# Optimization experiments

Hardware: AMD Instinct MI355X
Metric: run time of the kernel (lower is better)

Reference implementation:

```python
import jax, jax.numpy as jnp
import numpy as np
import math

B, S, D, H = 16, 1024, 768, 8
DK = D // H


def setup_inputs() -> dict:
    key = jax.random.key(0)
    ks = jax.random.split(key, 12)
    scale = 1.0 / math.sqrt(D)
    inp = {
        "query": jax.random.normal(ks[0], (B, S, D), jnp.float32),
        "key": jax.random.normal(ks[1], (B, S, D), jnp.float32),
        "value": jax.random.normal(ks[2], (B, S, D), jnp.float32),
        # 4 structured group masks (between/self/global/question), 0/1
        "mask": jax.random.randint(ks[3], (B, 4, S, S), 0, 2, jnp.int32),
        "Wq": jax.random.normal(ks[4], (D, D), jnp.float32) * scale,
        "bq": jnp.zeros((D,), jnp.float32),
        "Wk": jax.random.normal(ks[5], (D, D), jnp.float32) * scale,
        "bk": jnp.zeros((D,), jnp.float32),
        "Wv": jax.random.normal(ks[6], (D, D), jnp.float32) * scale,
        "bv": jnp.zeros((D,), jnp.float32),
        "Wo": jax.random.normal(ks[7], (D, D), jnp.float32) * scale,
        "bo": jnp.zeros((D,), jnp.float32),
    }
    return inp


def _split_heads(x):  # [B,S,D] -> [B,H,S,DK]
    b, s, _ = x.shape
    return x.reshape(b, s, H, DK).transpose(0, 2, 1, 3)


def reference(query, key, value, mask, Wq, bq, Wk, bk, Wv, bv, Wo, bo):
    # mask is 4-D -> torch code concatenates it with itself along dim 1: [B,8,S,S]
    m = jnp.concatenate([mask, mask], axis=1)
    q = _split_heads(query @ Wq.T + bq)
    k = _split_heads(key @ Wk.T + bk)
    v = _split_heads(value @ Wv.T + bv)
    scores = jnp.einsum("bhqd,bhkd->bhqk", q, k) / math.sqrt(DK)
    scores = jnp.where(m == 0, jnp.float32(-1e9), scores)
    p = jax.nn.softmax(scores, axis=-1)  # dropout = identity (eval mode)
    x = jnp.einsum("bhqk,bhkd->bhqd", p, v)
    x = x.transpose(0, 2, 1, 3).reshape(query.shape[0], -1, H * DK)
    return x @ Wo.T + bo
```

## Files before the change

kernel.cpp:

```cpp
#include <hip/hip_runtime.h>
#include <hip/hip_bf16.h>

typedef unsigned short u16;
typedef unsigned long long u64;
typedef __attribute__((ext_vector_type(4))) float f32x4;
typedef __attribute__((ext_vector_type(8))) short s16x8;

constexpr int Sdim = 1024;
constexpr int Hh   = 8;
constexpr int DKc  = 96;
constexpr int Dd   = 768;
constexpr int Bb   = 16;

static __device__ __forceinline__ u16 f2bf(float f) {
    unsigned u = __builtin_bit_cast(unsigned, f);
    u += 0x7fff + ((u >> 16) & 1);
    return (u16)(u >> 16);
}

__global__ __launch_bounds__(256) void convw_kernel(
    const float* w0, const float* w1, const float* w2, const float* w3, u16* dst)
{
    const float* src = (blockIdx.y == 0) ? w0 : (blockIdx.y == 1) ? w1
                      : (blockIdx.y == 2) ? w2 : w3;
    u16* d = dst + (size_t)blockIdx.y * 589824;
    int i = (blockIdx.x * 256 + threadIdx.x) * 4;
    float4 v = *(const float4*)(src + i);
    ushort4 o;
    o.x = f2bf(v.x); o.y = f2bf(v.y); o.z = f2bf(v.z); o.w = f2bf(v.w);
    *(ushort4*)(d + i) = o;
}

__global__ __launch_bounds__(256) void maskpack_kernel(const int* mask, unsigned* packed)
{
    const size_t total  = (size_t)Bb * 4 * Sdim * Sdim;
    const size_t stride = (size_t)gridDim.x * 256;
    const int lane = threadIdx.x & 63;
    for (size_t i = (size_t)blockIdx.x * 256 + threadIdx.x; i < total; i += stride) {
        int mv = mask[i];
        u64 bal = __ballot(mv != 0);
        size_t w0 = (i - lane) >> 5;
        if (lane == 0)  packed[w0]     = (unsigned)bal;
        if (lane == 32) packed[w0 + 1] = (unsigned)(bal >> 32);
    }
}

template<bool QKV>
__global__ __launch_bounds__(256) void gemm_kernel(
    const float* q_f32, const float* k_f32, const float* v_f32,
    const u16* xb, const u16* wb,
    const float* bq, const float* bk, const float* bv, const float* bo,
    u16* qb, u16* kb, u16* vtb, float* out, int Ktot)
{
    constexpr int LDT = 72;
    __shared__ u16 As[128][LDT];
    __shared__ u16 Bs[128][LDT];

    const int z = QKV ? (int)blockIdx.z : 3;
    const float* Af = QKV ? (z == 0 ? q_f32 : z == 1 ? k_f32 : v_f32) : nullptr;
    const u16*   Ab = QKV ? nullptr : xb;
    const u16*   W  = wb + (size_t)(QKV ? z : 3) * 589824;
    const float* bias = QKV ? (z == 0 ? bq : z == 1 ? bk : bv) : bo;

    const int tid = threadIdx.x;
    const int lane = tid & 63;
    const int w = tid >> 6;
    const int wr = (w >> 1) * 64, wc = (w & 1) * 64;
    const int m0 = blockIdx.y * 128, n0 = blockIdx.x * 128;

    f32x4 acc[4][4] = {};

    for (int k0 = 0; k0 < Ktot; k0 += 64) {
        __syncthreads();
        if constexpr (QKV) {
            #pragma unroll
            for (int i = 0; i < 8; i++) {
                int c = tid + i * 256;
                int row = c >> 4, o4 = (c & 15) * 4;
                float4 v = *(const float4*)(Af + (size_t)(m0 + row) * Ktot + k0 + o4);
                ushort4 o;
                o.x = f2bf(v.x); o.y = f2bf(v.y); o.z = f2bf(v.z); o.w = f2bf(v.w);
                *(ushort4*)&As[row][o4] = o;
            }
        } else {
            #pragma unroll
            for (int i = 0; i < 4; i++) {
                int c = tid + i * 256;
                int row = c >> 3, o8 = (c & 7) * 8;
                *(int4*)&As[row][o8] =
                    *(const int4*)(Ab + (size_t)(m0 + row) * Ktot + k0 + o8);
            }
        }
        #pragma unroll
        for (int i = 0; i < 4; i++) {
            int c = tid + i * 256;
            int row = c >> 3, o8 = (c & 7) * 8;
            *(int4*)&Bs[row][o8] =
                *(const int4*)(W + (size_t)(n0 + row) * Ktot + k0 + o8);
        }
        __syncthreads();
        #pragma unroll
        for (int kk = 0; kk < 2; kk++) {
            s16x8 a[4], b[4];
            #pragma unroll
            for (int mi = 0; mi < 4; mi++)
                a[mi] = *(const s16x8*)&As[wr + mi * 16 + (lane & 15)][kk * 32 + (lane >> 4) * 8];
            #pragma unroll
            for (int ni = 0; ni < 4; ni++)
                b[ni] = *(const s16x8*)&Bs[wc + ni * 16 + (lane & 15)][kk * 32 + (lane >> 4) * 8];
            #pragma unroll
            for (int mi = 0; mi < 4; mi++)
                #pragma unroll
                for (int ni = 0; ni < 4; ni++)
                    acc[mi][ni] = __builtin_amdgcn_mfma_f32_16x16x32_bf16(
                        a[mi], b[ni], acc[mi][ni], 0, 0, 0);
        }
    }

    #pragma unroll
    for (int mi = 0; mi < 4; mi++) {
        #pragma unroll
        for (int ni = 0; ni < 4; ni++) {
            int nc = n0 + wc + ni * 16 + (lane & 15);
            int mr0 = m0 + wr + mi * 16 + (lane >> 4) * 4;
            float bvv = bias[nc];
            float vals[4];
            #pragma unroll
            for (int r = 0; r < 4; r++) vals[r] = acc[mi][ni][r] + bvv;

            if constexpr (!QKV) {
                #pragma unroll
                for (int r = 0; r < 4; r++)
                    out[(size_t)(mr0 + r) * Dd + nc] = vals[r];
            } else {
                int b_ = mr0 >> 10, s_ = mr0 & 1023;
                int h_ = nc / DKc, dk = nc - h_ * DKc;
                if (z == 2) {
                    ushort4 o;
                    o.x = f2bf(vals[0]); o.y = f2bf(vals[1]);
                    o.z = f2bf(vals[2]); o.w = f2bf(vals[3]);
                    *(ushort4*)&vtb[((size_t)(b_ * Hh + h_) * DKc + dk) * Sdim + s_] = o;
                } else {
                    u16* dst = (z == 0) ? qb : kb;
                    #pragma unroll
                    for (int r = 0; r < 4; r++)
                        dst[((size_t)(b_ * Hh + h_) * Sdim + (s_ + r)) * DKc + dk] = f2bf(vals[r]);
                }
            }
        }
    }
}

__global__ __launch_bounds__(256) void attn_kernel(
    const u16* qb, const u16* kb, const u16* vtb, const unsigned* mpacked, u16* xb)
{
    __shared__ u16 kbuf[64][104];
    __shared__ u16 vbuf[96][72];
    __shared__ u16 pbuf[4][16][72];

    const int tid = threadIdx.x;
    const int lane = tid & 63;
    const int w = tid >> 6;
    const int bh = blockIdx.y;
    const int b_ = bh >> 3, h_ = bh & 7, g_ = h_ & 3;
    const int q0 = blockIdx.x * 64;

    const u16* Qp = qb + (size_t)bh * Sdim * DKc;
    const u16* Kp = kb + (size_t)bh * Sdim * DKc;
    const u16* Vp = vtb + (size_t)bh * DKc * Sdim;
    const unsigned* Pm = mpacked + (((size_t)(b_ * 4 + g_) * Sdim * Sdim) >> 5);

    #pragma unroll
    for (int i = 0; i < 3; i++) {
        int c = tid + i * 256;
        int row = c / 12, o = (c % 12) * 8;
        *(int4*)&kbuf[row][o] = *(const int4*)(Qp + (size_t)(q0 + row) * DKc + o);
    }
    __syncthreads();
    s16x8 qf[3];
    #pragma unroll
    for (int kk = 0; kk < 3; kk++)
        qf[kk] = *(const s16x8*)&kbuf[w * 16 + (lane & 15)][kk * 32 + (lane >> 4) * 8];
    __syncthreads();

    float m_run[4], l_run[4];
    f32x4 acc[6];
    #pragma unroll
    for (int r = 0; r < 4; r++) { m_run[r] = -1e30f; l_run[r] = 0.f; }
    #pragma unroll
    for (int n2 = 0; n2 < 6; n2++) acc[n2] = (f32x4){0.f, 0.f, 0.f, 0.f};

    const float sc = 0.10206207261596575f;
    const int qrow = q0 + w * 16 + (lane >> 4) * 4;

    for (int kt = 0; kt < 16; kt++) {
        const int kb0 = kt * 64;
        __syncthreads();
        #pragma unroll
        for (int i = 0; i < 3; i++) {
            int c = tid + i * 256;
            int row = c / 12, o = (c % 12) * 8;
            *(int4*)&kbuf[row][o] = *(const int4*)(Kp + (size_t)(kb0 + row) * DKc + o);
        }
        #pragma unroll
        for (int i = 0; i < 3; i++) {
            int c = tid + i * 256;
            int row = c >> 3, o = (c & 7) * 8;
            *(int4*)&vbuf[row][o] = *(const int4*)(Vp + (size_t)row * Sdim + kb0 + o);
        }
        __syncthreads();

        float s[4][4];
        #pragma unroll
        for (int ni = 0; ni < 4; ni++) {
            f32x4 c4 = {0.f, 0.f, 0.f, 0.f};
            #pragma unroll
            for (int kk = 0; kk < 3; kk++) {
                s16x8 bfr = *(const s16x8*)&kbuf[ni * 16 + (lane & 15)][kk * 32 + (lane >> 4) * 8];
                c4 = __builtin_amdgcn_mfma_f32_16x16x32_bf16(qf[kk], bfr, c4, 0, 0, 0);
            }
            #pragma unroll
            for (int r = 0; r < 4; r++) s[ni][r] = c4[r] * sc;
        }

        #pragma unroll
        for (int r = 0; r < 4; r++) {
            u64 mbits = *(const u64*)(Pm + (((size_t)(qrow + r) * Sdim + kb0) >> 5));
            #pragma unroll
            for (int ni = 0; ni < 4; ni++)
                if (!((mbits >> (ni * 16 + (lane & 15))) & 1)) s[ni][r] = -1e9f;
        }

        float alpha[4];
        #pragma unroll
        for (int r = 0; r < 4; r++) {
            float tmax = fmaxf(fmaxf(s[0][r], s[1][r]), fmaxf(s[2][r], s[3][r]));
            tmax = fmaxf(tmax, __shfl_xor(tmax, 1));
            tmax = fmaxf(tmax, __shfl_xor(tmax, 2));
            tmax = fmaxf(tmax, __shfl_xor(tmax, 4));
            tmax = fmaxf(tmax, __shfl_xor(tmax, 8));
            float mn = fmaxf(m_run[r], tmax);
            alpha[r] = __expf(m_run[r] - mn);
            m_run[r] = mn;
            float ps = 0.f;
            #pragma unroll
            for (int ni = 0; ni < 4; ni++) {
                float p = __expf(s[ni][r] - mn);
                s[ni][r] = p;
                ps += p;
            }
            ps += __shfl_xor(ps, 1);
            ps += __shfl_xor(ps, 2);
            ps += __shfl_xor(ps, 4);
            ps += __shfl_xor(ps, 8);
            l_run[r] = l_run[r] * alpha[r] + ps;
        }

        #pragma unroll
        for (int ni = 0; ni < 4; ni++)
            #pragma unroll
            for (int r = 0; r < 4; r++)
                pbuf[w][(lane >> 4) * 4 + r][ni * 16 + (lane & 15)] = f2bf(s[ni][r]);
        #pragma unroll
        for (int n2 = 0; n2 < 6; n2++)
            #pragma unroll
            for (int r = 0; r < 4; r++) acc[n2][r] *= alpha[r];
        asm volatile("s_waitcnt lgkmcnt(0)" ::: "memory");

        #pragma unroll
        for (int kk = 0; kk < 2; kk++) {
            s16x8 pf = *(const s16x8*)&pbuf[w][lane & 15][kk * 32 + (lane >> 4) * 8];
            #pragma unroll
            for (int n2 = 0; n2 < 6; n2++) {
                s16x8 vf = *(const s16x8*)&vbuf[n2 * 16 + (lane & 15)][kk * 32 + (lane >> 4) * 8];
                acc[n2] = __builtin_amdgcn_mfma_f32_16x16x32_bf16(pf, vf, acc[n2], 0, 0, 0);
            }
        }
    }

    #pragma unroll
    for (int n2 = 0; n2 < 6; n2++) {
        int dc = h_ * DKc + n2 * 16 + (lane & 15);
        #pragma unroll
        for (int r = 0; r < 4; r++) {
            float val = acc[n2][r] / l_run[r];
            xb[((size_t)(b_ * Sdim) + (qrow + r)) * Dd + dc] = f2bf(val);
        }
    }
}

extern "C" void kernel_launch(void* const* d_in, const int* in_sizes, int n_in,
                              void* d_out, int out_size, void* d_ws, size_t ws_size,
                              hipStream_t stream)
{
    const float* query = (const float*)d_in[0];
    const float* key   = (const float*)d_in[1];
    const float* value = (const float*)d_in[2];
    const int*   mask  = (const int*)d_in[3];
    const float* Wq = (const float*)d_in[4];
    const float* bq = (const float*)d_in[5];
    const float* Wk = (const float*)d_in[6];
    const float* bk = (const float*)d_in[7];
    const float* Wv = (const float*)d_in[8];
    const float* bv = (const float*)d_in[9];
    const float* Wo = (const float*)d_in[10];
    const float* bo = (const float*)d_in[11];
    float* out = (float*)d_out;

    char* ws = (char*)d_ws;
    u16* qb   = (u16*)(ws);
    u16* kb   = (u16*)(ws + 25165824);
    u16* vtb  = (u16*)(ws + 50331648);
    u16* xb   = (u16*)(ws + 75497472);
    u16* wb   = (u16*)(ws + 100663296);
    unsigned* mp = (unsigned*)(ws + 105381888);

    convw_kernel<<<dim3(576, 4), 256, 0, stream>>>(Wq, Wk, Wv, Wo, wb);
    maskpack_kernel<<<dim3(2048), 256, 0, stream>>>(mask, mp);
    gemm_kernel<true><<<dim3(6, 128, 3), 256, 0, stream>>>(
        query, key, value, nullptr, wb, bq, bk, bv, bo, qb, kb, vtb, out, Dd);
    attn_kernel<<<dim3(16, 128), 256, 0, stream>>>(qb, kb, vtb, mp, xb);
    gemm_kernel<false><<<dim3(6, 128, 1), 256, 0, stream>>>(
        nullptr, nullptr, nullptr, xb, wb, bq, bk, bv, bo, qb, kb, vtb, out, Dd);
}
```

Before: 828.4 us.

## Transpose QK^T tile, add lazy softmax rescale, and use direct-to-LDS GEMM loads

The attention kernel now computes S^T via swapped MFMA operands, so each lane owns a single query row. Row max and sum need only two cross-lane shuffles instead of four per row, and each lane loads one 64-bit mask word per tile. Softmax switches to exp2 with a pre-scaled log2e factor, skips accumulator rescaling unless the max grows by more than 8, and packs P to bf16 with v_cvt_pk_bf16_f32. The GEMM loads weight and bf16 activation tiles with global_load_lds into unpadded LDS, which may add bank conflicts on the fragment reads.

```diff
diff --git a/kernel.cpp b/kernel.cpp
--- a/kernel.cpp
+++ b/kernel.cpp
@@ -2,6 +2,7 @@
 #include <hip/hip_bf16.h>
 
 typedef unsigned short u16;
+typedef unsigned int u32;
 typedef unsigned long long u64;
 typedef __attribute__((ext_vector_type(4))) float f32x4;
 typedef __attribute__((ext_vector_type(8))) short s16x8;
@@ -16,6 +17,12 @@
     unsigned u = __builtin_bit_cast(unsigned, f);
     u += 0x7fff + ((u >> 16) & 1);
     return (u16)(u >> 16);
+}
+
+static __device__ __forceinline__ void gload_lds16(const u16* g, u16* l) {
+    __builtin_amdgcn_global_load_lds(
+        (const __attribute__((address_space(1))) u32*)g,
+        (__attribute__((address_space(3))) u32*)l, 16, 0, 0);
 }
 
 __global__ __launch_bounds__(256) void convw_kernel(
@@ -52,9 +59,9 @@
     const float* bq, const float* bk, const float* bv, const float* bo,
     u16* qb, u16* kb, u16* vtb, float* out, int Ktot)
 {
-    constexpr int LDT = 72;
-    __shared__ u16 As[128][LDT];
-    __shared__ u16 Bs[128][LDT];
+    constexpr int LDA = QKV ? 72 : 64;
+    __shared__ u16 As[128][LDA];
+    __shared__ u16 Bs[128][64];
 
     const int z = QKV ? (int)blockIdx.z : 3;
     const float* Af = QKV ? (z == 0 ? q_f32 : z == 1 ? k_f32 : v_f32) : nullptr;
@@ -72,6 +79,13 @@
 
     for (int k0 = 0; k0 < Ktot; k0 += 64) {
         __syncthreads();
+        #pragma unroll
+        for (int i = 0; i < 4; i++) {
+            int c = (w * 4 + i) * 64 + lane;
+            int row = c >> 3, col = (c & 7) * 8;
+            gload_lds16(W + (size_t)(n0 + row) * Ktot + k0 + col,
+                        ((u16*)Bs) + (size_t)(w * 4 + i) * 512);
+        }
         if constexpr (QKV) {
             #pragma unroll
             for (int i = 0; i < 8; i++) {
@@ -85,18 +99,11 @@
         } else {
             #pragma unroll
             for (int i = 0; i < 4; i++) {
-                int c = tid + i * 256;
-                int row = c >> 3, o8 = (c & 7) * 8;
-                *(int4*)&As[row][o8] =
-                    *(const int4*)(Ab + (size_t)(m0 + row) * Ktot + k0 + o8);
-            }
-        }
-        #pragma unroll
-        for (int i = 0; i < 4; i++) {
-            int c = tid + i * 256;
-            int row = c >> 3, o8 = (c & 7) * 8;
-            *(int4*)&Bs[row][o8] =
-                *(const int4*)(W + (size_t)(n0 + row) * Ktot + k0 + o8);
+                int c = (w * 4 + i) * 64 + lane;
+                int row = c >> 3, col = (c & 7) * 8;
+                gload_lds16(Ab + (size_t)(m0 + row) * Ktot + k0 + col,
+                            ((u16*)As) + (size_t)(w * 4 + i) * 512);
+            }
         }
         __syncthreads();
         #pragma unroll
@@ -161,6 +168,7 @@
     const int tid = threadIdx.x;
     const int lane = tid & 63;
     const int w = tid >> 6;
+    const int g = lane >> 4, g4 = g * 4, qll = lane & 15;
     const int bh = blockIdx.y;
     const int b_ = bh >> 3, h_ = bh & 7, g_ = h_ & 3;
     const int q0 = blockIdx.x * 64;
@@ -168,7 +176,8 @@
     const u16* Qp = qb + (size_t)bh * Sdim * DKc;
     const u16* Kp = kb + (size_t)bh * Sdim * DKc;
     const u16* Vp = vtb + (size_t)bh * DKc * Sdim;
-    const unsigned* Pm = mpacked + (((size_t)(b_ * 4 + g_) * Sdim * Sdim) >> 5);
+    const u64* mrow = (const u64*)(mpacked + (((size_t)(b_ * 4 + g_) * Sdim * Sdim) >> 5))
+                      + (size_t)(q0 + w * 16 + qll) * 16;
 
     #pragma unroll
     for (int i = 0; i < 3; i++) {
@@ -180,18 +189,15 @@
     s16x8 qf[3];
     #pragma unroll
     for (int kk = 0; kk < 3; kk++)
-        qf[kk] = *(const s16x8*)&kbuf[w * 16 + (lane & 15)][kk * 32 + (lane >> 4) * 8];
+        qf[kk] = *(const s16x8*)&kbuf[w * 16 + qll][kk * 32 + g * 8];
     __syncthreads();
 
-    float m_run[4], l_run[4];
+    float m_run = -1e30f, l_run = 0.f;
     f32x4 acc[6];
     #pragma unroll
-    for (int r = 0; r < 4; r++) { m_run[r] = -1e30f; l_run[r] = 0.f; }
-    #pragma unroll
     for (int n2 = 0; n2 < 6; n2++) acc[n2] = (f32x4){0.f, 0.f, 0.f, 0.f};
 
-    const float sc = 0.10206207261596575f;
-    const int qrow = q0 + w * 16 + (lane >> 4) * 4;
+    const float sc2 = 0.14724444609f;
 
     for (int kt = 0; kt < 16; kt++) {
         const int kb0 = kt * 64;
@@ -208,6 +214,7 @@
             int row = c >> 3, o = (c & 7) * 8;
             *(int4*)&vbuf[row][o] = *(const int4*)(Vp + (size_t)row * Sdim + kb0 + o);
         }
+        u64 mbits = mrow[kt];
         __syncthreads();
 
         float s[4][4];
@@ -216,75 +223,89 @@
             f32x4 c4 = {0.f, 0.f, 0.f, 0.f};
             #pragma unroll
             for (int kk = 0; kk < 3; kk++) {
-                s16x8 bfr = *(const s16x8*)&kbuf[ni * 16 + (lane & 15)][kk * 32 + (lane >> 4) * 8];
-                c4 = __builtin_amdgcn_mfma_f32_16x16x32_bf16(qf[kk], bfr, c4, 0, 0, 0);
-            }
-            #pragma unroll
-            for (int r = 0; r < 4; r++) s[ni][r] = c4[r] * sc;
-        }
-
-        #pragma unroll
-        for (int r = 0; r < 4; r++) {
-            u64 mbits = *(const u64*)(Pm + (((size_t)(qrow + r) * Sdim + kb0) >> 5));
-            #pragma unroll
-            for (int ni = 0; ni < 4; ni++)
-                if (!((mbits >> (ni * 16 + (lane & 15))) & 1)) s[ni][r] = -1e9f;
-        }
-
-        float alpha[4];
-        #pragma unroll
-        for (int r = 0; r < 4; r++) {
-            float tmax = fmaxf(fmaxf(s[0][r], s[1][r]), fmaxf(s[2][r], s[3][r]));
-            tmax = fmaxf(tmax, __shfl_xor(tmax, 1));
-            tmax = fmaxf(tmax, __shfl_xor(tmax, 2));
-            tmax = fmaxf(tmax, __shfl_xor(tmax, 4));
-            tmax = fmaxf(tmax, __shfl_xor(tmax, 8));
-            float mn = fmaxf(m_run[r], tmax);
-            alpha[r] = __expf(m_run[r] - mn);
-            m_run[r] = mn;
-            float ps = 0.f;
-            #pragma unroll
-            for (int ni = 0; ni < 4; ni++) {
-                float p = __expf(s[ni][r] - mn);
+                s16x8 kf = *(const s16x8*)&kbuf[ni * 16 + qll][kk * 32 + g * 8];
+                c4 = __builtin_amdgcn_mfma_f32_16x16x32_bf16(kf, qf[kk], c4, 0, 0, 0);
+            }
+            #pragma unroll
+            for (int r = 0; r < 4; r++) s[ni][r] = c4[r] * sc2;
+        }
+
+        #pragma unroll
+        for (int ni = 0; ni < 4; ni++) {
+            u32 mb = (u32)(mbits >> (ni * 16 + g4));
+            #pragma unroll
+            for (int r = 0; r < 4; r++)
+                if (!((mb >> r) & 1)) s[ni][r] = -1e9f;
+        }
+
+        float tmax = s[0][0];
+        #pragma unroll
+        for (int ni = 0; ni < 4; ni++)
+            #pragma unroll
+            for (int r = 0; r < 4; r++) tmax = fmaxf(tmax, s[ni][r]);
+        tmax = fmaxf(tmax, __shfl_xor(tmax, 16));
+        tmax = fmaxf(tmax, __shfl_xor(tmax, 32));
+
+        bool rescale = !__all(tmax <= m_run + 8.f);
+        float alpha = 1.f;
+        if (rescale) {
+            float mn = fmaxf(m_run, tmax);
+            alpha = exp2f(m_run - mn);
+            m_run = mn;
+        }
+        float ps = 0.f;
+        #pragma unroll
+        for (int ni = 0; ni < 4; ni++)
+            #pragma unroll
+            for (int r = 0; r < 4; r++) {
+                float p = exp2f(s[ni][r] - m_run);
                 s[ni][r] = p;
                 ps += p;
             }
-            ps += __shfl_xor(ps, 1);
-            ps += __shfl_xor(ps, 2);
-            ps += __shfl_xor(ps, 4);
-            ps += __shfl_xor(ps, 8);
-            l_run[r] = l_run[r] * alpha[r] + ps;
-        }
-
-        #pragma unroll
-        for (int ni = 0; ni < 4; ni++)
-            #pragma unroll
-            for (int r = 0; r < 4; r++)
-                pbuf[w][(lane >> 4) * 4 + r][ni * 16 + (lane & 15)] = f2bf(s[ni][r]);
-        #pragma unroll
-        for (int n2 = 0; n2 < 6; n2++)
-            #pragma unroll
-            for (int r = 0; r < 4; r++) acc[n2][r] *= alpha[r];
+        ps += __shfl_xor(ps, 16);
+        ps += __shfl_xor(ps, 32);
+        l_run = l_run * alpha + ps;
+
+        if (rescale) {
+            float ac[4];
+            #pragma unroll
+            for (int r = 0; r < 4; r++) ac[r] = __shfl(alpha, g4 + r, 16);
+            #pragma unroll
+            for (int n2 = 0; n2 < 6; n2++)
+                #pragma unroll
+                for (int r = 0; r < 4; r++) acc[n2][r] *= ac[r];
+        }
+
+        #pragma unroll
+        for (int ni = 0; ni < 4; ni++) {
+            u32 lo, hi;
+            asm("v_cvt_pk_bf16_f32 %0, %1, %2" : "=v"(lo) : "v"(s[ni][0]), "v"(s[ni][1]));
+            asm("v_cvt_pk_bf16_f32 %0, %1, %2" : "=v"(hi) : "v"(s[ni][2]), "v"(s[ni][3]));
+            *(uint2*)&pbuf[w][qll][ni * 16 + g4] = make_uint2(lo, hi);
+        }
         asm volatile("s_waitcnt lgkmcnt(0)" ::: "memory");
 
         #pragma unroll
         for (int kk = 0; kk < 2; kk++) {
-            s16x8 pf = *(const s16x8*)&pbuf[w][lane & 15][kk * 32 + (lane >> 4) * 8];
+            s16x8 pf = *(const s16x8*)&pbuf[w][qll][kk * 32 + g * 8];
             #pragma unroll
             for (int n2 = 0; n2 < 6; n2++) {
-                s16x8 vf = *(const s16x8*)&vbuf[n2 * 16 + (lane & 15)][kk * 32 + (lane >> 4) * 8];
+                s16x8 vf = *(const s16x8*)&vbuf[n2 * 16 + qll][kk * 32 + g * 8];
                 acc[n2] = __builtin_amdgcn_mfma_f32_16x16x32_bf16(pf, vf, acc[n2], 0, 0, 0);
             }
         }
     }
 
+    float il[4];
+    #pragma unroll
+    for (int r = 0; r < 4; r++) il[r] = 1.f / __shfl(l_run, g4 + r, 16);
     #pragma unroll
     for (int n2 = 0; n2 < 6; n2++) {
-        int dc = h_ * DKc + n2 * 16 + (lane & 15);
+        int dc = h_ * DKc + n2 * 16 + qll;
         #pragma unroll
         for (int r = 0; r < 4; r++) {
-            float val = acc[n2][r] / l_run[r];
-            xb[((size_t)(b_ * Sdim) + (qrow + r)) * Dd + dc] = f2bf(val);
+            int qrow_c = q0 + w * 16 + g4 + r;
+            xb[((size_t)(b_ * Sdim) + qrow_c) * Dd + dc] = f2bf(acc[n2][r] * il[r]);
         }
     }
 }
```

New measurement: 810.9 us. -2.1%, faster.
